# Performance work log

Hardware: AMD Instinct MI355X
Metric: run time of the kernel (lower is better)

## Reference

```python
import jax, jax.numpy as jnp
import numpy as np

NX, NU, NY = 128, 64, 32
N = 262144          # batch of state/input samples
GAMMA = 1.0
EPS = 1e-4          # self.eps in the torch module


def _psd_sqrtm(M):
    # differentiable matrix square root for a symmetric PSD matrix
    w, V = jnp.linalg.eigh(M)
    return (V * jnp.sqrt(jnp.clip(w, 0.0))) @ V.T


def setup_inputs() -> dict:
    key = jax.random.key(0)
    ks = jax.random.split(key, 7)
    u = jax.random.normal(ks[0], (N, NU), jnp.float32)
    x = jax.random.normal(ks[1], (N, NX), jnp.float32)
    # geotorch positive_definite(Q), positive_definite(P): materialize PSD matrices
    Mq = jax.random.normal(ks[2], (NX, NX), jnp.float32) / np.float32(np.sqrt(NX))
    Q = Mq @ Mq.T + 1e-2 * jnp.eye(NX, dtype=jnp.float32)
    Mp = jax.random.normal(ks[3], (NX, NX), jnp.float32) / np.float32(np.sqrt(NX))
    P = Mp @ Mp.T + 1e-2 * jnp.eye(NX, dtype=jnp.float32)
    # geotorch skew(S)
    Ms = jax.random.normal(ks[4], (NX, NX), jnp.float32)
    S = 0.5 * (Ms - Ms.T)
    G = jax.random.normal(ks[5], (NY, NX), jnp.float32)
    H = jax.random.normal(ks[6], (NX, NU), jnp.float32)
    return {"u": u, "x": x, "Q": Q, "P": P, "S": S, "G": G, "H": H}


def reference(u, x, Q, P, S, G, H):
    # Htilde = H / (1.01 * sqrt(||H H^T||_2)), spectral norm
    denom = 1.01 * jnp.sqrt(jnp.linalg.norm(H @ H.T, ord=2))
    Htilde = H / denom
    I = jnp.eye(NX, dtype=Q.dtype)
    Asym = -0.5 * (Q + G.T @ G + EPS * I)
    A = (Asym + S) @ P                      # (nx, nx)
    B = GAMMA * (_psd_sqrtm(Q) @ Htilde)    # (nx, nu)
    C = G @ P                               # (ny, nx)
    dx = x @ A.T + u @ B.T                  # (N, nx)
    y = x @ C.T                             # (N, ny)
    return dx, y
```

## Files before the change

### kernel.cpp

```cpp
#include <hip/hip_runtime.h>
#include <hip/hip_bf16.h>


#define NB 262144

typedef __attribute__((ext_vector_type(8))) short s8v;
typedef __attribute__((ext_vector_type(4))) short s4v;
typedef __attribute__((ext_vector_type(4))) float f4v;

__device__ __forceinline__ float bf2f(unsigned short s) {
  unsigned int u = ((unsigned int)s) << 16;
  return __uint_as_float(u);
}
__device__ __forceinline__ unsigned short f2bf(float f) {
  unsigned int u = __float_as_uint(f);
  u += 0x7fffu + ((u >> 16) & 1u);
  return (unsigned short)(u >> 16);
}

__global__ __launch_bounds__(256) void k_prep1(
    const float* __restrict__ Q, const float* __restrict__ S,
    const float* __restrict__ G, const float* __restrict__ H,
    float* __restrict__ Mf, float* __restrict__ HtH, unsigned short* __restrict__ W)
{
  const int bid = blockIdx.x, tid = threadIdx.x;
  if (bid < 64) {
    const int idx = bid * 256 + tid;
    const int j = idx >> 7, k = idx & 127;
    float g = 0.f;
    #pragma unroll 4
    for (int i = 0; i < 32; ++i)
      g += G[i * 128 + j] * G[i * 128 + k];
    Mf[idx] = -0.5f * (Q[idx] + g + ((j == k) ? 1e-4f : 0.f)) + S[idx];
  } else {
    const int e = (bid - 64) * 256 + tid;
    const int a = e >> 6, b = e & 63;
    float s = 0.f;
    #pragma unroll 4
    for (int r = 0; r < 128; ++r)
      s += H[r * 64 + a] * H[r * 64 + b];
    HtH[e] = s;
    if (bid == 64) {
      for (int i = 0; i < 8; ++i) {
        int e2 = i * 256 + tid;
        int n = 128 + (e2 >> 6), kk = 128 + (e2 & 63);
        W[n * 192 + kk] = 0;
      }
    }
  }
}

__global__ __launch_bounds__(256) void k_prepAC(
    const float* __restrict__ Mf, const float* __restrict__ P,
    const float* __restrict__ G, unsigned short* __restrict__ W)
{
  const int bid = blockIdx.x, tid = threadIdx.x;
  if (bid < 64) {
    const int idx = bid * 256 + tid;
    const int n = idx >> 7, k = idx & 127;
    float s = 0.f;
    #pragma unroll 4
    for (int l = 0; l < 128; ++l)
      s += Mf[n * 128 + l] * P[l * 128 + k];
    W[n * 192 + k] = f2bf(s);
  } else {
    for (int i = 0; i < 4; ++i) {
      int e = (bid - 64) * 1024 + i * 256 + tid;
      int j = e >> 7, k = e & 127;
      float s = 0.f;
      #pragma unroll 4
      for (int l = 0; l < 128; ++l)
        s += G[j * 128 + l] * P[l * 128 + k];
      W[(128 + j) * 192 + k] = f2bf(s);
    }
  }
}

__global__ __launch_bounds__(1024) void k_prep23(
    const float* __restrict__ Qg, const float* __restrict__ Hg,
    const float* __restrict__ HtHg, unsigned short* __restrict__ W)
{
  __shared__ char smem[65536];
  unsigned short* Xs = (unsigned short*)smem;
  unsigned short* V0s = (unsigned short*)(smem + 32768);
  unsigned short* V1s = (unsigned short*)(smem + 49152);
  float* vQ = (float*)(smem + 32768);
  float* wQ = (float*)(smem + 33280);
  float* vH = (float*)(smem + 33792);
  float* wH = (float*)(smem + 34048);
  float* red = (float*)(smem + 34304);
  float* HtHs = (float*)(smem + 49152);

  const int tid = threadIdx.x;
  const int lane = tid & 63;
  const int wv = tid >> 6;

  for (int i = 0; i < 16; ++i) {
    int e = i * 1024 + tid;
    int m = e >> 7, k = e & 127;
    Xs[m * 128 + (((k >> 3) ^ (m & 7)) << 3) + (k & 7)] = f2bf(Qg[e]);
  }
  for (int i = 0; i < 4; ++i) HtHs[i * 1024 + tid] = HtHg[i * 1024 + tid] * 0.00390625f;
  if (tid < 128) vQ[tid] = (float)((tid * 1103515245u + 12345u) & 0xffffu) * (1.f / 65536.f) + 0.05f;
  if (tid < 64)  vH[tid] = (float)((tid * 2654435761u + 911u) & 0xffffu) * (1.f / 65536.f) + 0.05f;
  __syncthreads();

  float* qin = vQ; float* qout = wQ;
  float* hin = vH; float* hout = wH;
  for (int it = 0; it < 32; ++it) {
    if (tid < 512) {
      const int row = tid >> 2, sub = tid & 3;
      float p = 0.f;
      #pragma unroll
      for (int c = 0; c < 4; ++c) {
        const int ch = sub * 4 + c;
        const s8v q = *(const s8v*)&Xs[row * 128 + ((ch ^ (row & 7)) << 3)];
        const f4v a = *(const f4v*)&qin[ch * 8];
        const f4v b = *(const f4v*)&qin[ch * 8 + 4];
        p += bf2f((unsigned short)q[0]) * a[0];
        p += bf2f((unsigned short)q[1]) * a[1];
        p += bf2f((unsigned short)q[2]) * a[2];
        p += bf2f((unsigned short)q[3]) * a[3];
        p += bf2f((unsigned short)q[4]) * b[0];
        p += bf2f((unsigned short)q[5]) * b[1];
        p += bf2f((unsigned short)q[6]) * b[2];
        p += bf2f((unsigned short)q[7]) * b[3];
      }
      p += __shfl_xor(p, 1); p += __shfl_xor(p, 2);
      if (it == 16) p *= 0x1p-32f;
      if (sub == 0) qout[row] = p;
    } else {
      const int idx = tid - 512;
      const int row = idx >> 3, sub = idx & 7;
      const f4v a  = *(const f4v*)&HtHs[row * 64 + sub * 8];
      const f4v b  = *(const f4v*)&HtHs[row * 64 + sub * 8 + 4];
      const f4v va = *(const f4v*)&hin[sub * 8];
      const f4v vb = *(const f4v*)&hin[sub * 8 + 4];
      float p = a[0] * va[0] + a[1] * va[1] + a[2] * va[2] + a[3] * va[3]
              + b[0] * vb[0] + b[1] * vb[1] + b[2] * vb[2] + b[3] * vb[3];
      p += __shfl_xor(p, 1); p += __shfl_xor(p, 2); p += __shfl_xor(p, 4);
      if (it == 16) p *= 0x1p-8f;
      if (sub == 0) hout[row] = p;
    }
    __syncthreads();
    float* t;
    t = qin; qin = qout; qout = t;
    t = hin; hin = hout; hout = t;
  }

  {
    float s = 0.f;
    if (wv == 0)      { float a = qin[lane],  b = qin[lane + 64];  s = a * a + b * b; }
    else if (wv == 1) { float a = qout[lane], b = qout[lane + 64]; s = a * a + b * b; }
    else if (wv == 2) { float a = hin[lane];  s = a * a; }
    else if (wv == 3) { float a = hout[lane]; s = a * a; }
    if (wv < 4) {
      s += __shfl_xor(s, 1); s += __shfl_xor(s, 2); s += __shfl_xor(s, 4);
      s += __shfl_xor(s, 8); s += __shfl_xor(s, 16); s += __shfl_xor(s, 32);
      if (lane == 0) red[wv] = s;
    }
  }
  __syncthreads();
  if (tid == 0) {
    red[4] = sqrtf(red[0] / red[1]);
    red[5] = 256.f * sqrtf(red[2] / red[3]);
  }
  __syncthreads();
  const float bb = 1.10f * red[4];
  const float sqrtb = sqrtf(bb);
  const float invden = 1.f / (1.01f * sqrtf(red[5]));
  __syncthreads();

  for (int i = 0; i < 16; ++i) {
    int e = i * 1024 + tid;
    int m = e >> 7, k = e & 127;
    int a = m * 128 + (((k >> 3) ^ (m & 7)) << 3) + (k & 7);
    float q = bf2f(Xs[a]);
    Xs[a] = f2bf(q * (2.f / bb) - ((m == k) ? 1.f : 0.f));
  }
  for (int i = 0; i < 8; ++i) {
    int e = i * 1024 + tid;
    int j = e & 63, m = e >> 6;
    V0s[j * 128 + (((m >> 3) ^ (j & 7)) << 3) + (m & 7)] = f2bf(Hg[m * 64 + j] * invden);
  }
  const int t0 = wv * 2;
  float baccR[2][4];
  #pragma unroll
  for (int tt = 0; tt < 2; ++tt) {
    int mt = (t0 + tt) >> 2, nt = (t0 + tt) & 3;
    int n = nt * 16 + (lane & 15);
    int mb = mt * 16 + ((lane >> 4) << 2);
    #pragma unroll
    for (int i = 0; i < 4; ++i)
      baccR[tt][i] = 0.63661977f * Hg[(mb + i) * 64 + n] * invden;
  }
  __syncthreads();

  unsigned short* Vc = V0s;
  unsigned short* Vp = V1s;
  for (int k = 1; k <= 32; ++k) {
    const float ck = ((k & 1) ? 1.0f : -1.0f) / (3.14159265f * ((float)(k * k) - 0.25f));
    #pragma unroll
    for (int tt = 0; tt < 2; ++tt) {
      const int mt = (t0 + tt) >> 2, nt = (t0 + tt) & 3;
      f4v acc = {0.f, 0.f, 0.f, 0.f};
      const int arow = mt * 16 + (lane & 15);
      const int brow = nt * 16 + (lane & 15);
      #pragma unroll
      for (int ks = 0; ks < 4; ++ks) {
        int kc = ks * 4 + (lane >> 4);
        s8v af = *(const s8v*)&Xs[arow * 128 + ((kc ^ (arow & 7)) << 3)];
        s8v bf = *(const s8v*)&Vc[brow * 128 + ((kc ^ (brow & 7)) << 3)];
        acc = __builtin_amdgcn_mfma_f32_16x16x32_bf16(af, bf, acc, 0, 0, 0);
      }
      const int n = brow;
      const int mb = mt * 16 + ((lane >> 4) << 2);
      const int vaddr = n * 128 + (((mb >> 3) ^ (n & 7)) << 3) + (mb & 7);
      float nv[4];
      if (k == 1) {
        #pragma unroll
        for (int i = 0; i < 4; ++i) nv[i] = acc[i];
      } else {
        s4v ov = *(const s4v*)&Vp[vaddr];
        #pragma unroll
        for (int i = 0; i < 4; ++i) nv[i] = 2.f * acc[i] - bf2f((unsigned short)ov[i]);
      }
      s4v st;
      #pragma unroll
      for (int i = 0; i < 4; ++i) { st[i] = (short)f2bf(nv[i]); baccR[tt][i] += ck * nv[i]; }
      *(s4v*)&Vp[vaddr] = st;
    }
    __syncthreads();
    unsigned short* t = Vc; Vc = Vp; Vp = t;
  }

  #pragma unroll
  for (int tt = 0; tt < 2; ++tt) {
    const int mt = (t0 + tt) >> 2, nt = (t0 + tt) & 3;
    const int n = nt * 16 + (lane & 15);
    const int mb = mt * 16 + ((lane >> 4) << 2);
    #pragma unroll
    for (int i = 0; i < 4; ++i)
      W[(mb + i) * 192 + 128 + n] = f2bf(sqrtb * baccR[tt][i]);
  }
}

__global__ __launch_bounds__(256, 3) void k_main(
    const float* __restrict__ x, const float* __restrict__ u,
    const unsigned short* __restrict__ W, float* __restrict__ out)
{
  __shared__ char smraw[128 * 200 * 2];
  unsigned short* sm = (unsigned short*)smraw;
  float* fb = (float*)smraw;

  const int tid = threadIdx.x, lane = tid & 63, w = tid >> 6;
  const int mw = w & 1, nw = w >> 1;
  const int base = blockIdx.x * 128;

  s8v wf[5][6];
  {
    const int n0 = nw * 80 + (lane & 15);
    const int kof = (lane >> 4) * 8;
    #pragma unroll
    for (int nt = 0; nt < 5; ++nt)
      #pragma unroll
      for (int ks = 0; ks < 6; ++ks)
        wf[nt][ks] = *(const s8v*)&W[(n0 + nt * 16) * 192 + ks * 32 + kof];
  }
  #pragma unroll
  for (int p = 0; p < 16; ++p) {
    int g = p * 256 + tid; int r = g >> 5, c = g & 31;
    f4v v = *(const f4v*)&x[(size_t)(base + r) * 128 + c * 4];
    s4v b;
    #pragma unroll
    for (int i = 0; i < 4; ++i) b[i] = (short)f2bf(v[i]);
    *(s4v*)&sm[r * 200 + c * 4] = b;
  }
  #pragma unroll
  for (int p = 0; p < 8; ++p) {
    int g = p * 256 + tid; int r = g >> 4, c = g & 15;
    f4v v = *(const f4v*)&u[(size_t)(base + r) * 64 + c * 4];
    s4v b;
    #pragma unroll
    for (int i = 0; i < 4; ++i) b[i] = (short)f2bf(v[i]);
    *(s4v*)&sm[r * 200 + 128 + c * 4] = b;
  }
  __syncthreads();

  f4v acc[4][5];
  #pragma unroll
  for (int mt = 0; mt < 4; ++mt)
    #pragma unroll
    for (int nt = 0; nt < 5; ++nt)
      acc[mt][nt] = (f4v){0.f, 0.f, 0.f, 0.f};

  #pragma unroll
  for (int mt = 0; mt < 4; ++mt) {
    const int row = mw * 64 + mt * 16 + (lane & 15);
    const int kof = (lane >> 4) * 8;
    #pragma unroll
    for (int ks = 0; ks < 6; ++ks) {
      s8v af = *(const s8v*)&sm[row * 200 + ks * 32 + kof];
      #pragma unroll
      for (int nt = 0; nt < 5; ++nt)
        acc[mt][nt] = __builtin_amdgcn_mfma_f32_16x16x32_bf16(af, wf[nt][ks], acc[mt][nt], 0, 0, 0);
    }
  }

  float* const yout = out + (size_t)NB * 128;
  #pragma unroll
  for (int pass = 0; pass < 2; ++pass) {
    __syncthreads();
    if (mw == pass) {
      #pragma unroll
      for (int mt = 0; mt < 4; ++mt)
        #pragma unroll
        for (int nt = 0; nt < 5; ++nt) {
          const int rr = mt * 16 + ((lane >> 4) << 2);
          const int cc = nw * 80 + nt * 16 + (lane & 15);
          #pragma unroll
          for (int i = 0; i < 4; ++i)
            fb[(rr + i) * 164 + cc] = acc[mt][nt][i];
        }
    }
    __syncthreads();
    const int rb = base + pass * 64;
    #pragma unroll
    for (int p = 0; p < 8; ++p) {
      int g = p * 256 + tid; int r = g >> 5, c = g & 31;
      *(f4v*)&out[(size_t)(rb + r) * 128 + c * 4] = *(const f4v*)&fb[r * 164 + c * 4];
    }
    #pragma unroll
    for (int p = 0; p < 2; ++p) {
      int g = p * 256 + tid; int r = g >> 3, c = g & 7;
      *(f4v*)&yout[(size_t)(rb + r) * 32 + c * 4] = *(const f4v*)&fb[r * 164 + 128 + c * 4];
    }
  }
}

extern "C" void kernel_launch(void* const* d_in, const int* in_sizes, int n_in,
                              void* d_out, int out_size, void* d_ws, size_t ws_size,
                              hipStream_t stream) {
  const float *u = nullptr, *x = nullptr, *G = nullptr, *H = nullptr;
  const float* sq[3] = {nullptr, nullptr, nullptr};
  int nsq = 0;
  for (int i = 0; i < n_in; ++i) {
    const float* p = (const float*)d_in[i];
    switch (in_sizes[i]) {
      case NB * 64:  u = p; break;
      case NB * 128: x = p; break;
      case 32 * 128: G = p; break;
      case 128 * 64: H = p; break;
      case 128 * 128: if (nsq < 3) sq[nsq++] = p; break;
      default: break;
    }
  }
  const float* Q = sq[0];
  const float* P = sq[1];
  const float* S = sq[2];

  char* ws = (char*)d_ws;
  unsigned short* W = (unsigned short*)ws;
  float* HtH = (float*)(ws + 61440);
  float* Mf  = (float*)(ws + 77824);
  float* out = (float*)d_out;

  k_prep1 <<<80,   256,  0, stream>>>(Q, S, G, H, Mf, HtH, W);
  k_prepAC<<<68,   256,  0, stream>>>(Mf, P, G, W);
  k_prep23<<<1,    1024, 0, stream>>>(Q, H, HtH, W);
  k_main  <<<2048, 256,  0, stream>>>(x, u, W, out);
}
```

Measured before the change: 492.1 us.

## Make main GEMM kernel persistent with double-buffered register prefetch of next tile

Replaces the 2048-block one-shot kernel with a 512-block persistent loop over 64-row tiles. Each iteration prefetches the next tile's x/u into registers while computing MFMAs on the current tile, then converts and stores it into the other LDS buffer. This amortizes the per-block weight-fragment loads and overlaps global loads with compute and stores. The cost is more register pressure (occupancy hint lowered to 2) and smaller tiles per iteration.

New measurement: 456.1 us. 1.08x faster.

```diff
diff --git a/kernel.cpp b/kernel.cpp
--- a/kernel.cpp
+++ b/kernel.cpp
@@ -3,6 +3,9 @@
 
 
 #define NB 262144
+#define GRID 512
+#define TILES (NB / 64)
+#define ITERS (TILES / GRID)
 
 typedef __attribute__((ext_vector_type(8))) short s8v;
 typedef __attribute__((ext_vector_type(4))) short s4v;
@@ -245,96 +248,139 @@
   }
 }
 
-__global__ __launch_bounds__(256, 3) void k_main(
+__global__ __launch_bounds__(256, 2) void k_main(
     const float* __restrict__ x, const float* __restrict__ u,
     const unsigned short* __restrict__ W, float* __restrict__ out)
 {
-  __shared__ char smraw[128 * 200 * 2];
-  unsigned short* sm = (unsigned short*)smraw;
-  float* fb = (float*)smraw;
+  __shared__ char smraw[2][64 * 200 * 2];
 
   const int tid = threadIdx.x, lane = tid & 63, w = tid >> 6;
   const int mw = w & 1, nw = w >> 1;
-  const int base = blockIdx.x * 128;
-
+  float* const yout = out + (size_t)NB * 128;
+
+  const int n0 = nw * 80 + (lane & 15);
+  const int kof = (lane >> 4) * 8;
   s8v wf[5][6];
+  #pragma unroll
+  for (int nt = 0; nt < 5; ++nt)
+    #pragma unroll
+    for (int ks = 0; ks < 6; ++ks)
+      wf[nt][ks] = *(const s8v*)&W[(n0 + nt * 16) * 192 + ks * 32 + kof];
+
   {
-    const int n0 = nw * 80 + (lane & 15);
-    const int kof = (lane >> 4) * 8;
-    #pragma unroll
-    for (int nt = 0; nt < 5; ++nt)
-      #pragma unroll
-      for (int ks = 0; ks < 6; ++ks)
-        wf[nt][ks] = *(const s8v*)&W[(n0 + nt * 16) * 192 + ks * 32 + kof];
-  }
-  #pragma unroll
-  for (int p = 0; p < 16; ++p) {
-    int g = p * 256 + tid; int r = g >> 5, c = g & 31;
-    f4v v = *(const f4v*)&x[(size_t)(base + r) * 128 + c * 4];
-    s4v b;
-    #pragma unroll
-    for (int i = 0; i < 4; ++i) b[i] = (short)f2bf(v[i]);
-    *(s4v*)&sm[r * 200 + c * 4] = b;
-  }
-  #pragma unroll
-  for (int p = 0; p < 8; ++p) {
-    int g = p * 256 + tid; int r = g >> 4, c = g & 15;
-    f4v v = *(const f4v*)&u[(size_t)(base + r) * 64 + c * 4];
-    s4v b;
-    #pragma unroll
-    for (int i = 0; i < 4; ++i) b[i] = (short)f2bf(v[i]);
-    *(s4v*)&sm[r * 200 + 128 + c * 4] = b;
-  }
-  __syncthreads();
-
-  f4v acc[4][5];
-  #pragma unroll
-  for (int mt = 0; mt < 4; ++mt)
-    #pragma unroll
-    for (int nt = 0; nt < 5; ++nt)
-      acc[mt][nt] = (f4v){0.f, 0.f, 0.f, 0.f};
-
-  #pragma unroll
-  for (int mt = 0; mt < 4; ++mt) {
-    const int row = mw * 64 + mt * 16 + (lane & 15);
-    const int kof = (lane >> 4) * 8;
-    #pragma unroll
-    for (int ks = 0; ks < 6; ++ks) {
-      s8v af = *(const s8v*)&sm[row * 200 + ks * 32 + kof];
-      #pragma unroll
-      for (int nt = 0; nt < 5; ++nt)
-        acc[mt][nt] = __builtin_amdgcn_mfma_f32_16x16x32_bf16(af, wf[nt][ks], acc[mt][nt], 0, 0, 0);
-    }
-  }
-
-  float* const yout = out + (size_t)NB * 128;
-  #pragma unroll
-  for (int pass = 0; pass < 2; ++pass) {
-    __syncthreads();
-    if (mw == pass) {
-      #pragma unroll
-      for (int mt = 0; mt < 4; ++mt)
-        #pragma unroll
-        for (int nt = 0; nt < 5; ++nt) {
-          const int rr = mt * 16 + ((lane >> 4) << 2);
-          const int cc = nw * 80 + nt * 16 + (lane & 15);
-          #pragma unroll
-          for (int i = 0; i < 4; ++i)
-            fb[(rr + i) * 164 + cc] = acc[mt][nt][i];
-        }
-    }
-    __syncthreads();
-    const int rb = base + pass * 64;
+    unsigned short* sm0 = (unsigned short*)smraw[0];
+    const int base = blockIdx.x * 64;
     #pragma unroll
     for (int p = 0; p < 8; ++p) {
       int g = p * 256 + tid; int r = g >> 5, c = g & 31;
-      *(f4v*)&out[(size_t)(rb + r) * 128 + c * 4] = *(const f4v*)&fb[r * 164 + c * 4];
-    }
-    #pragma unroll
-    for (int p = 0; p < 2; ++p) {
-      int g = p * 256 + tid; int r = g >> 3, c = g & 7;
-      *(f4v*)&yout[(size_t)(rb + r) * 32 + c * 4] = *(const f4v*)&fb[r * 164 + 128 + c * 4];
-    }
+      f4v v = *(const f4v*)&x[(size_t)(base + r) * 128 + c * 4];
+      s4v b;
+      #pragma unroll
+      for (int i = 0; i < 4; ++i) b[i] = (short)f2bf(v[i]);
+      *(s4v*)&sm0[r * 200 + c * 4] = b;
+    }
+    #pragma unroll
+    for (int p = 0; p < 4; ++p) {
+      int g = p * 256 + tid; int r = g >> 4, c = g & 15;
+      f4v v = *(const f4v*)&u[(size_t)(base + r) * 64 + c * 4];
+      s4v b;
+      #pragma unroll
+      for (int i = 0; i < 4; ++i) b[i] = (short)f2bf(v[i]);
+      *(s4v*)&sm0[r * 200 + 128 + c * 4] = b;
+    }
+  }
+  __syncthreads();
+
+  int cur = 0;
+  for (int it2 = 0; it2 < ITERS; ++it2) {
+    const int base = (blockIdx.x + it2 * GRID) * 64;
+    const bool hasnext = (it2 + 1 < ITERS);
+    const int nbase = (blockIdx.x + (it2 + 1) * GRID) * 64;
+
+    f4v px[8], pu[4];
+    if (hasnext) {
+      #pragma unroll
+      for (int p = 0; p < 8; ++p) {
+        int g = p * 256 + tid; int r = g >> 5, c = g & 31;
+        px[p] = *(const f4v*)&x[(size_t)(nbase + r) * 128 + c * 4];
+      }
+      #pragma unroll
+      for (int p = 0; p < 4; ++p) {
+        int g = p * 256 + tid; int r = g >> 4, c = g & 15;
+        pu[p] = *(const f4v*)&u[(size_t)(nbase + r) * 64 + c * 4];
+      }
+    }
+
+    unsigned short* sm = (unsigned short*)smraw[cur];
+    f4v acc[2][5];
+    #pragma unroll
+    for (int mt = 0; mt < 2; ++mt)
+      #pragma unroll
+      for (int nt = 0; nt < 5; ++nt)
+        acc[mt][nt] = (f4v){0.f, 0.f, 0.f, 0.f};
+
+    const int row0 = mw * 32 + (lane & 15);
+    #pragma unroll
+    for (int ks = 0; ks < 6; ++ks) {
+      s8v af0 = *(const s8v*)&sm[(row0     ) * 200 + ks * 32 + kof];
+      s8v af1 = *(const s8v*)&sm[(row0 + 16) * 200 + ks * 32 + kof];
+      #pragma unroll
+      for (int nt = 0; nt < 5; ++nt) {
+        acc[0][nt] = __builtin_amdgcn_mfma_f32_16x16x32_bf16(af0, wf[nt][ks], acc[0][nt], 0, 0, 0);
+        acc[1][nt] = __builtin_amdgcn_mfma_f32_16x16x32_bf16(af1, wf[nt][ks], acc[1][nt], 0, 0, 0);
+      }
+    }
+
+    float* fb = (float*)smraw[cur];
+    #pragma unroll
+    for (int pass = 0; pass < 2; ++pass) {
+      __syncthreads();
+      if (mw == pass) {
+        #pragma unroll
+        for (int mt = 0; mt < 2; ++mt)
+          #pragma unroll
+          for (int nt = 0; nt < 5; ++nt) {
+            const int rr = mt * 16 + ((lane >> 4) << 2);
+            const int cc = nw * 80 + nt * 16 + (lane & 15);
+            #pragma unroll
+            for (int i = 0; i < 4; ++i)
+              fb[(rr + i) * 164 + cc] = acc[mt][nt][i];
+          }
+      }
+      __syncthreads();
+      const int rb = base + pass * 32;
+      #pragma unroll
+      for (int p = 0; p < 4; ++p) {
+        int g = p * 256 + tid; int r = g >> 5, c = g & 31;
+        *(f4v*)&out[(size_t)(rb + r) * 128 + c * 4] = *(const f4v*)&fb[r * 164 + c * 4];
+      }
+      {
+        int r = tid >> 3, c = tid & 7;
+        *(f4v*)&yout[(size_t)(rb + r) * 32 + c * 4] = *(const f4v*)&fb[r * 164 + 128 + c * 4];
+      }
+    }
+
+    if (hasnext) {
+      unsigned short* smn = (unsigned short*)smraw[cur ^ 1];
+      #pragma unroll
+      for (int p = 0; p < 8; ++p) {
+        int g = p * 256 + tid; int r = g >> 5, c = g & 31;
+        s4v b;
+        #pragma unroll
+        for (int i = 0; i < 4; ++i) b[i] = (short)f2bf(px[p][i]);
+        *(s4v*)&smn[r * 200 + c * 4] = b;
+      }
+      #pragma unroll
+      for (int p = 0; p < 4; ++p) {
+        int g = p * 256 + tid; int r = g >> 4, c = g & 15;
+        s4v b;
+        #pragma unroll
+        for (int i = 0; i < 4; ++i) b[i] = (short)f2bf(pu[p][i]);
+        *(s4v*)&smn[r * 200 + 128 + c * 4] = b;
+      }
+    }
+    __syncthreads();
+    cur ^= 1;
   }
 }
 
@@ -368,5 +414,5 @@
   k_prep1 <<<80,   256,  0, stream>>>(Q, S, G, H, Mf, HtH, W);
   k_prepAC<<<68,   256,  0, stream>>>(Mf, P, G, W);
   k_prep23<<<1,    1024, 0, stream>>>(Q, H, HtH, W);
-  k_main  <<<2048, 256,  0, stream>>>(x, u, W, out);
-}
+  k_main  <<<GRID, 256,  0, stream>>>(x, u, W, out);
+}
```

## Remove LDS staging in main GEMM and load/store global memory directly

Applied to the files above, without the earlier changes.

The main kernel no longer stages x/u into shared memory or writes outputs through a shared-memory buffer. Each wave now loads its MFMA A-fragments straight from global memory and converts them to bf16 in registers, then writes accumulators directly to dx/y. The block covers 64 rows instead of 128, the grid doubles to 4096, and the launch bound is relaxed to 2 blocks per SM. This drops the barriers and LDS traffic but produces less coalesced global access, with scattered 4-byte stores and 32-byte row reads.

After: 464.9 us. -5.5%, faster.

```diff
diff --git a/kernel.cpp b/kernel.cpp
--- a/kernel.cpp
+++ b/kernel.cpp
@@ -245,95 +245,71 @@
   }
 }
 
-__global__ __launch_bounds__(256, 3) void k_main(
+__global__ __launch_bounds__(256, 2) void k_main(
     const float* __restrict__ x, const float* __restrict__ u,
     const unsigned short* __restrict__ W, float* __restrict__ out)
 {
-  __shared__ char smraw[128 * 200 * 2];
-  unsigned short* sm = (unsigned short*)smraw;
-  float* fb = (float*)smraw;
-
   const int tid = threadIdx.x, lane = tid & 63, w = tid >> 6;
   const int mw = w & 1, nw = w >> 1;
-  const int base = blockIdx.x * 128;
+  const int base = blockIdx.x * 64;
+  float* const yout = out + (size_t)NB * 128;
+
+  const int n0 = nw * 80 + (lane & 15);
+  const int kof = (lane >> 4) * 8;
 
   s8v wf[5][6];
-  {
-    const int n0 = nw * 80 + (lane & 15);
-    const int kof = (lane >> 4) * 8;
-    #pragma unroll
-    for (int nt = 0; nt < 5; ++nt)
-      #pragma unroll
-      for (int ks = 0; ks < 6; ++ks)
-        wf[nt][ks] = *(const s8v*)&W[(n0 + nt * 16) * 192 + ks * 32 + kof];
-  }
-  #pragma unroll
-  for (int p = 0; p < 16; ++p) {
-    int g = p * 256 + tid; int r = g >> 5, c = g & 31;
-    f4v v = *(const f4v*)&x[(size_t)(base + r) * 128 + c * 4];
-    s4v b;
-    #pragma unroll
-    for (int i = 0; i < 4; ++i) b[i] = (short)f2bf(v[i]);
-    *(s4v*)&sm[r * 200 + c * 4] = b;
-  }
-  #pragma unroll
-  for (int p = 0; p < 8; ++p) {
-    int g = p * 256 + tid; int r = g >> 4, c = g & 15;
-    f4v v = *(const f4v*)&u[(size_t)(base + r) * 64 + c * 4];
-    s4v b;
-    #pragma unroll
-    for (int i = 0; i < 4; ++i) b[i] = (short)f2bf(v[i]);
-    *(s4v*)&sm[r * 200 + 128 + c * 4] = b;
-  }
-  __syncthreads();
-
-  f4v acc[4][5];
-  #pragma unroll
-  for (int mt = 0; mt < 4; ++mt)
+  #pragma unroll
+  for (int nt = 0; nt < 5; ++nt)
+    #pragma unroll
+    for (int ks = 0; ks < 6; ++ks)
+      wf[nt][ks] = *(const s8v*)&W[(n0 + nt * 16) * 192 + ks * 32 + kof];
+
+  f4v acc[2][5];
+  #pragma unroll
+  for (int mt = 0; mt < 2; ++mt)
     #pragma unroll
     for (int nt = 0; nt < 5; ++nt)
       acc[mt][nt] = (f4v){0.f, 0.f, 0.f, 0.f};
 
   #pragma unroll
-  for (int mt = 0; mt < 4; ++mt) {
-    const int row = mw * 64 + mt * 16 + (lane & 15);
-    const int kof = (lane >> 4) * 8;
+  for (int mt = 0; mt < 2; ++mt) {
+    const int rowg = base + mw * 32 + mt * 16 + (lane & 15);
+    const float* __restrict__ xrow = x + (size_t)rowg * 128;
+    const float* __restrict__ urow = u + (size_t)rowg * 64;
     #pragma unroll
     for (int ks = 0; ks < 6; ++ks) {
-      s8v af = *(const s8v*)&sm[row * 200 + ks * 32 + kof];
+      f4v v0, v1;
+      if (ks < 4) {
+        v0 = *(const f4v*)&xrow[ks * 32 + kof];
+        v1 = *(const f4v*)&xrow[ks * 32 + kof + 4];
+      } else {
+        v0 = *(const f4v*)&urow[(ks - 4) * 32 + kof];
+        v1 = *(const f4v*)&urow[(ks - 4) * 32 + kof + 4];
+      }
+      s8v af;
+      #pragma unroll
+      for (int i = 0; i < 4; ++i) { af[i] = (short)f2bf(v0[i]); af[4 + i] = (short)f2bf(v1[i]); }
       #pragma unroll
       for (int nt = 0; nt < 5; ++nt)
         acc[mt][nt] = __builtin_amdgcn_mfma_f32_16x16x32_bf16(af, wf[nt][ks], acc[mt][nt], 0, 0, 0);
     }
   }
 
-  float* const yout = out + (size_t)NB * 128;
-  #pragma unroll
-  for (int pass = 0; pass < 2; ++pass) {
-    __syncthreads();
-    if (mw == pass) {
-      #pragma unroll
-      for (int mt = 0; mt < 4; ++mt)
+  #pragma unroll
+  for (int mt = 0; mt < 2; ++mt) {
+    const int grow = base + mw * 32 + mt * 16 + ((lane >> 4) << 2);
+    #pragma unroll
+    for (int nt = 0; nt < 5; ++nt) {
+      const int col = n0 + nt * 16;
+      if (col < 128) {
         #pragma unroll
-        for (int nt = 0; nt < 5; ++nt) {
-          const int rr = mt * 16 + ((lane >> 4) << 2);
-          const int cc = nw * 80 + nt * 16 + (lane & 15);
-          #pragma unroll
-          for (int i = 0; i < 4; ++i)
-            fb[(rr + i) * 164 + cc] = acc[mt][nt][i];
-        }
-    }
-    __syncthreads();
-    const int rb = base + pass * 64;
-    #pragma unroll
-    for (int p = 0; p < 8; ++p) {
-      int g = p * 256 + tid; int r = g >> 5, c = g & 31;
-      *(f4v*)&out[(size_t)(rb + r) * 128 + c * 4] = *(const f4v*)&fb[r * 164 + c * 4];
-    }
-    #pragma unroll
-    for (int p = 0; p < 2; ++p) {
-      int g = p * 256 + tid; int r = g >> 3, c = g & 7;
-      *(f4v*)&yout[(size_t)(rb + r) * 32 + c * 4] = *(const f4v*)&fb[r * 164 + 128 + c * 4];
+        for (int i = 0; i < 4; ++i)
+          out[(size_t)(grow + i) * 128 + col] = acc[mt][nt][i];
+      } else {
+        #pragma unroll
+        for (int i = 0; i < 4; ++i)
+          yout[(size_t)(grow + i) * 32 + (col - 128)] = acc[mt][nt][i];
+      }
     }
   }
 }
@@ -368,5 +344,5 @@
   k_prep1 <<<80,   256,  0, stream>>>(Q, S, G, H, Mf, HtH, W);
   k_prepAC<<<68,   256,  0, stream>>>(Mf, P, G, W);
   k_prep23<<<1,    1024, 0, stream>>>(Q, H, HtH, W);
-  k_main  <<<2048, 256,  0, stream>>>(x, u, W, out);
-}
+  k_main  <<<4096, 256,  0, stream>>>(x, u, W, out);
+}
```
